# Optimization experiments

Hardware: AMD Instinct MI355X
Metric: run time of the kernel (lower is better)

Reference implementation:

```python
import jax, jax.numpy as jnp
import numpy as np

DIMS = 2048
HEAD_DIM = 64
NUM_HEADS = DIMS // HEAD_DIM   # 32
GQA_HEADS = 2                  # KV heads
EPS = 1e-8


def setup_inputs() -> dict:
    key = jax.random.key(0)
    ks = jax.random.split(key, 6)
    b, s = 2, 2048
    kv_dims = HEAD_DIM * GQA_HEADS  # 128
    x = jax.random.normal(ks[0], (b, s, DIMS), dtype=jnp.float32)
    Wq = jax.random.normal(ks[1], (DIMS, DIMS), dtype=jnp.float32) * 0.02
    Wk = jax.random.normal(ks[2], (kv_dims, DIMS), dtype=jnp.float32) * 0.02
    Wv = jax.random.normal(ks[3], (kv_dims, DIMS), dtype=jnp.float32) * 0.02
    Wo = jax.random.normal(ks[4], (DIMS, DIMS), dtype=jnp.float32) * 0.02
    norm_scale = jnp.ones((DIMS,), dtype=jnp.float32)           # RMSNorm.scale
    split_scale = jnp.full((DIMS,), 0.1, dtype=jnp.float32)     # RMS_split.scale
    return {"x": x, "norm_scale": norm_scale, "split_scale": split_scale,
            "Wq": Wq, "Wk": Wk, "Wv": Wv, "Wo": Wo}


def reference(x, norm_scale, split_scale, Wq, Wk, Wv, Wo):
    b, s, d = x.shape
    H, G, dh = NUM_HEADS, GQA_HEADS, HEAD_DIM
    hpg = H // G  # query heads per KV group

    # RMS_split pre-norm: RMSNorm (l2-norm based) then elementwise scale
    nrm = jnp.linalg.norm(x, axis=-1, keepdims=True) * (d ** -0.5)
    h = (norm_scale * x / (nrm + EPS)) * split_scale

    # projections (nn.Linear with weight [out, in], no bias)
    q = (h @ Wq.T).reshape(b, s, H, dh)          # b s H dh
    k = (h @ Wk.T).reshape(b, s, G, dh)          # b s G dh
    v = (h @ Wv.T).reshape(b, s, G, dh)

    # group query heads: b G hpg s dh
    q = q.transpose(0, 2, 1, 3).reshape(b, G, hpg, s, dh)
    k = k.transpose(0, 2, 1, 3)                  # b G s dh
    v = v.transpose(0, 2, 1, 3)                  # b G s dh

    scores = jnp.einsum('bghsd,bgtd->bghst', q, k) / np.float32(np.sqrt(dh))
    attn = jax.nn.softmax(scores, axis=-1)
    out = jnp.einsum('bghst,bgtd->bghsd', attn, v)   # b G hpg s dh

    out = out.reshape(b, H, s, dh).transpose(0, 2, 1, 3).reshape(b, s, H * dh)
    return x + out @ Wo.T
```

## Files before the change

kernel.cpp:

```cpp
#include <hip/hip_runtime.h>

typedef unsigned short u16;
typedef unsigned int u32;
typedef __bf16 bf16x8 __attribute__((ext_vector_type(8)));
typedef float f32x4 __attribute__((ext_vector_type(4)));

#define DIMS 2048
#define SEQ 2048
#define BATCH 2
#define NH 32
#define NG 2
#define DH 64
#define MROWS (BATCH * SEQ)
#define KVD (NG * DH)

#define SCL2 (0.125f * 1.44269504088896f)

__device__ __forceinline__ u16 f2bf(float f) {
  u32 u = __float_as_uint(f);
  u32 r = u + 0x7fffu + ((u >> 16) & 1u);
  return (u16)(r >> 16);
}
__device__ __forceinline__ u32 pack2(float a, float b) {
  return (u32)f2bf(a) | ((u32)f2bf(b) << 16);
}
__device__ __forceinline__ u32 cvtpk(float a, float b) {
#if __has_builtin(__builtin_amdgcn_cvt_pk_bf16_f32)
  typedef __bf16 bf16x2 __attribute__((ext_vector_type(2)));
  union {
    bf16x2 v;
    u32 u;
  } r;
  r.v = __builtin_amdgcn_cvt_pk_bf16_f32(a, b);
  return r.u;
#else
  return pack2(a, b);
#endif
}
__device__ __forceinline__ void glds16(const u16* g, u16* l) {
  __builtin_amdgcn_global_load_lds(
      (const __attribute__((address_space(1))) void*)g,
      (__attribute__((address_space(3))) void*)l, 16, 0, 0);
}

__global__ __launch_bounds__(256) void rms_split_kernel(
    const float* __restrict__ x, const float* __restrict__ ns,
    const float* __restrict__ ss, u16* __restrict__ h) {
  const int row = blockIdx.x;
  const int tid = threadIdx.x;
  const float* xr = x + (size_t)row * DIMS;
  float4 v0 = ((const float4*)xr)[tid];
  float4 v1 = ((const float4*)xr)[tid + 256];
  float s = v0.x * v0.x + v0.y * v0.y + v0.z * v0.z + v0.w * v0.w +
            v1.x * v1.x + v1.y * v1.y + v1.z * v1.z + v1.w * v1.w;
#pragma unroll
  for (int d = 1; d < 64; d <<= 1) s += __shfl_xor(s, d, 64);
  __shared__ float red[4];
  if ((tid & 63) == 0) red[tid >> 6] = s;
  __syncthreads();
  float tot = red[0] + red[1] + red[2] + red[3];
  float inv = 1.0f / (sqrtf(tot * (1.0f / DIMS)) + 1e-8f);
  float4 a0 = ((const float4*)ns)[tid];
  float4 a1 = ((const float4*)ns)[tid + 256];
  float4 b0 = ((const float4*)ss)[tid];
  float4 b1 = ((const float4*)ss)[tid + 256];
  uint2 o0, o1;
  o0.x = pack2(v0.x * a0.x * b0.x * inv, v0.y * a0.y * b0.y * inv);
  o0.y = pack2(v0.z * a0.z * b0.z * inv, v0.w * a0.w * b0.w * inv);
  o1.x = pack2(v1.x * a1.x * b1.x * inv, v1.y * a1.y * b1.y * inv);
  o1.y = pack2(v1.z * a1.z * b1.z * inv, v1.w * a1.w * b1.w * inv);
  uint2* hr = (uint2*)(h + (size_t)row * DIMS);
  hr[tid] = o0;
  hr[tid + 256] = o1;
}

__global__ __launch_bounds__(256) void cvt4_kernel(
    const float* __restrict__ Wq, const float* __restrict__ Wo,
    const float* __restrict__ Wk, const float* __restrict__ Wv,
    u16* __restrict__ bqkv, u16* __restrict__ bWo) {
  const int bx = blockIdx.x;
  const float* src;
  u16* dst;
  int i;
  if (bx < 4096) {
    src = Wq; dst = bqkv; i = bx;
  } else if (bx < 8192) {
    src = Wo; dst = bWo; i = bx - 4096;
  } else if (bx < 8448) {
    src = Wk; dst = bqkv + (size_t)2048 * 2048; i = bx - 8192;
  } else {
    src = Wv; dst = bqkv + (size_t)2176 * 2048; i = bx - 8448;
  }
  const int idx = i * 256 + threadIdx.x;
  float4 v = ((const float4*)src)[idx];
  uint2 r;
  r.x = pack2(v.x, v.y);
  r.y = pack2(v.z, v.w);
  ((uint2*)dst)[idx] = r;
}

template <int MODE>
__global__ __launch_bounds__(256) void gemm_bt(
    const u16* __restrict__ A, const u16* __restrict__ B, void* __restrict__ Cv,
    const float* __restrict__ R, u16* __restrict__ kb, u16* __restrict__ vtb,
    int M, int N, int K) {
  __shared__ u16 As[2][128 * 32];
  __shared__ u16 Bs[2][128 * 32];
  const int tid = threadIdx.x;
  const int lane = tid & 63;
  const int wv = tid >> 6;
  const int fr = lane & 15;
  const int fq = lane >> 4;
  const int m0 = blockIdx.y * 128;
  const int n0 = blockIdx.x * 128;
  const int wm = wv & 1;
  const int wn = wv >> 1;

  const int srow = tid >> 2;
  const int scol = (tid & 3) * 8;
  const u16* Ag0 = A + (size_t)(m0 + srow) * K + scol;
  const u16* Ag1 = A + (size_t)(m0 + srow + 64) * K + scol;
  const u16* Bg0 = B + (size_t)(n0 + srow) * K + scol;
  const u16* Bg1 = B + (size_t)(n0 + srow + 64) * K + scol;

  f32x4 acc[4][4];
#pragma unroll
  for (int i = 0; i < 4; ++i)
#pragma unroll
    for (int j = 0; j < 4; ++j)
#pragma unroll
      for (int e = 0; e < 4; ++e) acc[i][j][e] = 0.0f;

#define GSTAGE(buf, kk)                            \
  {                                                \
    glds16(Ag0 + (kk), &As[buf][wv * 512]);        \
    glds16(Ag1 + (kk), &As[buf][2048 + wv * 512]); \
    glds16(Bg0 + (kk), &Bs[buf][wv * 512]);        \
    glds16(Bg1 + (kk), &Bs[buf][2048 + wv * 512]); \
  }

#define GCOMP(buf)                                                            \
  {                                                                           \
    bf16x8 af_[4], bf_[4];                                                    \
    _Pragma("unroll") for (int i = 0; i < 4; ++i) {                           \
      af_[i] = *(const bf16x8*)(&As[buf][(wm * 64 + i * 16 + fr) * 32 +       \
                                         fq * 8]);                            \
      bf_[i] = *(const bf16x8*)(&Bs[buf][(wn * 64 + i * 16 + fr) * 32 +       \
                                         fq * 8]);                            \
    }                                                                         \
    _Pragma("unroll") for (int i = 0; i < 4; ++i)                             \
        _Pragma("unroll") for (int j = 0; j < 4; ++j) acc[i][j] =             \
        __builtin_amdgcn_mfma_f32_16x16x32_bf16(af_[i], bf_[j], acc[i][j], 0, \
                                                0, 0);                        \
  }

  GSTAGE(0, 0);
  int k0 = 0;
  for (; k0 + 64 < K; k0 += 64) {
    GSTAGE(1, k0 + 32);
    asm volatile("s_waitcnt vmcnt(4)\ns_barrier" ::: "memory");
    GCOMP(0);
    asm volatile("s_barrier" ::: "memory");
    GSTAGE(0, k0 + 64);
    asm volatile("s_waitcnt vmcnt(4)\ns_barrier" ::: "memory");
    GCOMP(1);
    asm volatile("s_barrier" ::: "memory");
  }
  GSTAGE(1, k0 + 32);
  asm volatile("s_waitcnt vmcnt(4)\ns_barrier" ::: "memory");
  GCOMP(0);
  asm volatile("s_barrier" ::: "memory");
  asm volatile("s_waitcnt vmcnt(0)\ns_barrier" ::: "memory");
  GCOMP(1);
#undef GSTAGE
#undef GCOMP

#pragma unroll
  for (int i = 0; i < 4; ++i) {
    const int m = m0 + wm * 64 + i * 16 + fq * 4;
#pragma unroll
    for (int j = 0; j < 4; ++j) {
      const int n = n0 + wn * 64 + j * 16 + fr;
#pragma unroll
      for (int r = 0; r < 4; ++r) {
        if (MODE == 1) {
          const size_t idx = (size_t)(m + r) * N + n;
          ((float*)Cv)[idx] = R[idx] + acc[i][j][r];
        } else {
          if (n0 < 2048) {
            ((u16*)Cv)[(size_t)(m + r) * DIMS + n] = f2bf(acc[i][j][r]);
          } else {
            const int token = m + r;
            const int bb = token >> 11;
            const int srw = token & 2047;
            const int t = srw >> 6;
            const int rowin = srw & 63;
            if (n0 < 2176) {
              const int d = n - 2048;
              const int gg = d >> 6;
              const int dd = d & 63;
              const int c = ((dd >> 5) << 2) | ((dd >> 3) & 3);
              const int jj = dd & 7;
              const int pos = (rowin & 32) | ((rowin & 4) << 2) |
                              ((rowin & 0x18) >> 1) | (rowin & 3);
              kb[(((size_t)(bb * NG + gg) * 32 + t) * 8 + c) * 512 + pos * 8 +
                 jj] = f2bf(acc[i][j][r] * SCL2);
            } else {
              const int d = n - 2176;
              const int gg = d >> 6;
              const int dv = d & 63;
              const int c = rowin >> 3;
              const int jj = rowin & 7;
              vtb[(((size_t)(bb * NG + gg) * 32 + t) * 8 + c) * 512 + dv * 8 +
                  jj] = f2bf(acc[i][j][r]);
            }
          }
        }
      }
    }
  }
}

__global__ __launch_bounds__(256, 4) void attn_kernel(
    const u16* __restrict__ q, const u16* __restrict__ kbuf,
    const u16* __restrict__ vT, u16* __restrict__ out) {
  __shared__ u16 Ks[2][8 * 512];
  __shared__ u16 Vs[2][8 * 512];
  const int tid = threadIdx.x;
  const int lane = tid & 63;
  const int wv = tid >> 6;
  const int fr = lane & 15;
  const int fq = lane >> 4;
  const int b = blockIdx.x >> 5;
  const int hq = blockIdx.x & 31;
  const int g = hq >> 4;
  const int q0 = blockIdx.y * 128 + wv * 32;

  bf16x8 af[2][2];
#pragma unroll
  for (int mt = 0; mt < 2; ++mt)
#pragma unroll
    for (int kx = 0; kx < 2; ++kx)
      af[mt][kx] =
          *(const bf16x8*)(q + (size_t)(b * SEQ + q0 + mt * 16 + fr) * DIMS +
                           hq * DH + kx * 32 + fq * 8);

  f32x4 Oa[2][4];
  f32x4 On[2];
#pragma unroll
  for (int mt = 0; mt < 2; ++mt) {
#pragma unroll
    for (int e = 0; e < 4; ++e) On[mt][e] = 0.0f;
#pragma unroll
    for (int j = 0; j < 4; ++j)
#pragma unroll
      for (int e = 0; e < 4; ++e) Oa[mt][j][e] = 0.0f;
  }

  bf16x8 onev;
#pragma unroll
  for (int e = 0; e < 8; ++e) onev[e] = (__bf16)1.0f;

  const u16* ksrc = kbuf + (size_t)(b * NG + g) * 32 * 4096;
  const u16* vsrc = vT + (size_t)(b * NG + g) * 32 * 4096;

  const int c0 = wv * 2;
#define STAGE(buf, tile)                                          \
  {                                                               \
    const size_t tb_ = (size_t)(tile)*4096;                       \
    _Pragma("unroll") for (int s = 0; s < 2; ++s) {               \
      const int c = c0 + s;                                       \
      glds16(ksrc + tb_ + c * 512 + lane * 8, &Ks[buf][c * 512]); \
      glds16(vsrc + tb_ + c * 512 + lane * 8, &Vs[buf][c * 512]); \
    }                                                             \
  }

#define COMPUTE(buf)                                                          \
  {                                                                           \
    _Pragma("unroll") for (int kg = 0; kg < 2; ++kg) {                        \
      bf16x8 kf00 = *(const bf16x8*)(&Ks[buf][fq * 512 + (kg * 32 + fr) * 8]); \
      bf16x8 kf01 =                                                           \
          *(const bf16x8*)(&Ks[buf][(4 + fq) * 512 + (kg * 32 + fr) * 8]);    \
      bf16x8 kf10 =                                                           \
          *(const bf16x8*)(&Ks[buf][fq * 512 + (kg * 32 + 16 + fr) * 8]);     \
      bf16x8 kf11 = *(const bf16x8*)(&Ks[buf][(4 + fq) * 512 +                \
                                              (kg * 32 + 16 + fr) * 8]);      \
      bf16x8 vf[4];                                                           \
      _Pragma("unroll") for (int jt = 0; jt < 4; ++jt) vf[jt] =               \
          *(const bf16x8*)(&Vs[buf][(kg * 4 + fq) * 512 + (jt * 16 + fr) * 8]); \
      _Pragma("unroll") for (int mt = 0; mt < 2; ++mt) {                      \
        f32x4 s0 = {0.0f, 0.0f, 0.0f, 0.0f};                                  \
        f32x4 s1 = {0.0f, 0.0f, 0.0f, 0.0f};                                  \
        s0 = __builtin_amdgcn_mfma_f32_16x16x32_bf16(kf00, af[mt][0], s0, 0,  \
                                                     0, 0);                   \
        s0 = __builtin_amdgcn_mfma_f32_16x16x32_bf16(kf01, af[mt][1], s0, 0,  \
                                                     0, 0);                   \
        s1 = __builtin_amdgcn_mfma_f32_16x16x32_bf16(kf10, af[mt][0], s1, 0,  \
                                                     0, 0);                   \
        s1 = __builtin_amdgcn_mfma_f32_16x16x32_bf16(kf11, af[mt][1], s1, 0,  \
                                                     0, 0);                   \
        const float p0 = __builtin_amdgcn_exp2f(s0[0]);                       \
        const float p1 = __builtin_amdgcn_exp2f(s0[1]);                       \
        const float p2 = __builtin_amdgcn_exp2f(s0[2]);                       \
        const float p3 = __builtin_amdgcn_exp2f(s0[3]);                       \
        const float p4 = __builtin_amdgcn_exp2f(s1[0]);                       \
        const float p5 = __builtin_amdgcn_exp2f(s1[1]);                       \
        const float p6 = __builtin_amdgcn_exp2f(s1[2]);                       \
        const float p7 = __builtin_amdgcn_exp2f(s1[3]);                       \
        union {                                                               \
          bf16x8 v;                                                           \
          u32 u[4];                                                           \
        } pu;                                                                 \
        pu.u[0] = cvtpk(p0, p1);                                              \
        pu.u[1] = cvtpk(p2, p3);                                              \
        pu.u[2] = cvtpk(p4, p5);                                              \
        pu.u[3] = cvtpk(p6, p7);                                              \
        _Pragma("unroll") for (int jt = 0; jt < 4; ++jt) Oa[mt][jt] =         \
            __builtin_amdgcn_mfma_f32_16x16x32_bf16(pu.v, vf[jt], Oa[mt][jt], \
                                                    0, 0, 0);                 \
        On[mt] = __builtin_amdgcn_mfma_f32_16x16x32_bf16(pu.v, onev, On[mt],  \
                                                         0, 0, 0);            \
      }                                                                       \
    }                                                                         \
  }

  STAGE(0, 0);
  for (int it = 0; it < 32; it += 2) {
    STAGE(1, (it + 1) & 31);
    asm volatile("s_waitcnt vmcnt(4)\ns_barrier" ::: "memory");
    COMPUTE(0);
    asm volatile("s_barrier" ::: "memory");
    STAGE(0, (it + 2) & 31);
    asm volatile("s_waitcnt vmcnt(4)\ns_barrier" ::: "memory");
    COMPUTE(1);
    asm volatile("s_barrier" ::: "memory");
  }
#undef STAGE
#undef COMPUTE

#pragma unroll
  for (int mt = 0; mt < 2; ++mt)
#pragma unroll
    for (int r = 0; r < 4; ++r) {
      const float invl = 1.0f / On[mt][r];
      const int row = q0 + mt * 16 + fq * 4 + r;
#pragma unroll
      for (int jt = 0; jt < 4; ++jt)
        out[(size_t)(b * SEQ + row) * DIMS + hq * DH + jt * 16 + fr] =
            f2bf(Oa[mt][jt][r] * invl);
    }
}

extern "C" void kernel_launch(void* const* d_in, const int* in_sizes, int n_in,
                              void* d_out, int out_size, void* d_ws,
                              size_t ws_size, hipStream_t stream) {
  const float* x = (const float*)d_in[0];
  const float* ns = (const float*)d_in[1];
  const float* ssc = (const float*)d_in[2];
  const float* Wq = (const float*)d_in[3];
  const float* Wk = (const float*)d_in[4];
  const float* Wv = (const float*)d_in[5];
  const float* Wo = (const float*)d_in[6];

  char* ws = (char*)d_ws;
  u16* hbuf = (u16*)(ws);
  u16* bqkv = (u16*)(ws + 16777216);
  u16* bWo = (u16*)(ws + 26214400);
  u16* qb = (u16*)(ws + 34603008);
  u16* kb = (u16*)(ws + 51380224);
  u16* vtb = (u16*)(ws + 52428800);
  u16* ab = (u16*)(ws + 53477376);

  rms_split_kernel<<<dim3(4096), dim3(256), 0, stream>>>(x, ns, ssc, hbuf);
  cvt4_kernel<<<dim3(8704), dim3(256), 0, stream>>>(Wq, Wo, Wk, Wv, bqkv, bWo);

  gemm_bt<2><<<dim3(18, 32), dim3(256), 0, stream>>>(
      hbuf, bqkv, qb, nullptr, kb, vtb, 4096, 2048, 2048);
  attn_kernel<<<dim3(64, 16), dim3(256), 0, stream>>>(qb, kb, vtb, ab);
  gemm_bt<1><<<dim3(16, 32), dim3(256), 0, stream>>>(
      ab, bWo, d_out, x, nullptr, nullptr, 4096, 2048, 2048);
}
```

Before: 299.8 us.

## Widen GEMM K-tile with swizzled LDS, XCD block remap, fuse prep kernels

```diff
diff --git a/kernel.cpp b/kernel.cpp
--- a/kernel.cpp
+++ b/kernel.cpp
@@ -43,60 +43,60 @@
       (__attribute__((address_space(3))) void*)l, 16, 0, 0);
 }
 
-__global__ __launch_bounds__(256) void rms_split_kernel(
+__global__ __launch_bounds__(256) void prep_kernel(
     const float* __restrict__ x, const float* __restrict__ ns,
-    const float* __restrict__ ss, u16* __restrict__ h) {
-  const int row = blockIdx.x;
-  const int tid = threadIdx.x;
-  const float* xr = x + (size_t)row * DIMS;
-  float4 v0 = ((const float4*)xr)[tid];
-  float4 v1 = ((const float4*)xr)[tid + 256];
-  float s = v0.x * v0.x + v0.y * v0.y + v0.z * v0.z + v0.w * v0.w +
-            v1.x * v1.x + v1.y * v1.y + v1.z * v1.z + v1.w * v1.w;
-#pragma unroll
-  for (int d = 1; d < 64; d <<= 1) s += __shfl_xor(s, d, 64);
-  __shared__ float red[4];
-  if ((tid & 63) == 0) red[tid >> 6] = s;
-  __syncthreads();
-  float tot = red[0] + red[1] + red[2] + red[3];
-  float inv = 1.0f / (sqrtf(tot * (1.0f / DIMS)) + 1e-8f);
-  float4 a0 = ((const float4*)ns)[tid];
-  float4 a1 = ((const float4*)ns)[tid + 256];
-  float4 b0 = ((const float4*)ss)[tid];
-  float4 b1 = ((const float4*)ss)[tid + 256];
-  uint2 o0, o1;
-  o0.x = pack2(v0.x * a0.x * b0.x * inv, v0.y * a0.y * b0.y * inv);
-  o0.y = pack2(v0.z * a0.z * b0.z * inv, v0.w * a0.w * b0.w * inv);
-  o1.x = pack2(v1.x * a1.x * b1.x * inv, v1.y * a1.y * b1.y * inv);
-  o1.y = pack2(v1.z * a1.z * b1.z * inv, v1.w * a1.w * b1.w * inv);
-  uint2* hr = (uint2*)(h + (size_t)row * DIMS);
-  hr[tid] = o0;
-  hr[tid + 256] = o1;
-}
-
-__global__ __launch_bounds__(256) void cvt4_kernel(
+    const float* __restrict__ ss, u16* __restrict__ h,
     const float* __restrict__ Wq, const float* __restrict__ Wo,
     const float* __restrict__ Wk, const float* __restrict__ Wv,
     u16* __restrict__ bqkv, u16* __restrict__ bWo) {
   const int bx = blockIdx.x;
-  const float* src;
-  u16* dst;
-  int i;
+  const int tid = threadIdx.x;
   if (bx < 4096) {
-    src = Wq; dst = bqkv; i = bx;
-  } else if (bx < 8192) {
-    src = Wo; dst = bWo; i = bx - 4096;
-  } else if (bx < 8448) {
-    src = Wk; dst = bqkv + (size_t)2048 * 2048; i = bx - 8192;
+    const float* xr = x + (size_t)bx * DIMS;
+    float4 v0 = ((const float4*)xr)[tid];
+    float4 v1 = ((const float4*)xr)[tid + 256];
+    float s = v0.x * v0.x + v0.y * v0.y + v0.z * v0.z + v0.w * v0.w +
+              v1.x * v1.x + v1.y * v1.y + v1.z * v1.z + v1.w * v1.w;
+#pragma unroll
+    for (int d = 1; d < 64; d <<= 1) s += __shfl_xor(s, d, 64);
+    __shared__ float red[4];
+    if ((tid & 63) == 0) red[tid >> 6] = s;
+    __syncthreads();
+    float tot = red[0] + red[1] + red[2] + red[3];
+    float inv = 1.0f / (sqrtf(tot * (1.0f / DIMS)) + 1e-8f);
+    float4 a0 = ((const float4*)ns)[tid];
+    float4 a1 = ((const float4*)ns)[tid + 256];
+    float4 b0 = ((const float4*)ss)[tid];
+    float4 b1 = ((const float4*)ss)[tid + 256];
+    uint2 o0, o1;
+    o0.x = pack2(v0.x * a0.x * b0.x * inv, v0.y * a0.y * b0.y * inv);
+    o0.y = pack2(v0.z * a0.z * b0.z * inv, v0.w * a0.w * b0.w * inv);
+    o1.x = pack2(v1.x * a1.x * b1.x * inv, v1.y * a1.y * b1.y * inv);
+    o1.y = pack2(v1.z * a1.z * b1.z * inv, v1.w * a1.w * b1.w * inv);
+    uint2* hr = (uint2*)(h + (size_t)bx * DIMS);
+    hr[tid] = o0;
+    hr[tid + 256] = o1;
   } else {
-    src = Wv; dst = bqkv + (size_t)2176 * 2048; i = bx - 8448;
-  }
-  const int idx = i * 256 + threadIdx.x;
-  float4 v = ((const float4*)src)[idx];
-  uint2 r;
-  r.x = pack2(v.x, v.y);
-  r.y = pack2(v.z, v.w);
-  ((uint2*)dst)[idx] = r;
+    const int cx = bx - 4096;
+    const float* src;
+    u16* dst;
+    int i;
+    if (cx < 4096) {
+      src = Wq; dst = bqkv; i = cx;
+    } else if (cx < 8192) {
+      src = Wo; dst = bWo; i = cx - 4096;
+    } else if (cx < 8448) {
+      src = Wk; dst = bqkv + (size_t)2048 * 2048; i = cx - 8192;
+    } else {
+      src = Wv; dst = bqkv + (size_t)2176 * 2048; i = cx - 8448;
+    }
+    const int idx = i * 256 + tid;
+    float4 v = ((const float4*)src)[idx];
+    uint2 r;
+    r.x = pack2(v.x, v.y);
+    r.y = pack2(v.z, v.w);
+    ((uint2*)dst)[idx] = r;
+  }
 }
 
 template <int MODE>
@@ -104,24 +104,34 @@
     const u16* __restrict__ A, const u16* __restrict__ B, void* __restrict__ Cv,
     const float* __restrict__ R, u16* __restrict__ kb, u16* __restrict__ vtb,
     int M, int N, int K) {
-  __shared__ u16 As[2][128 * 32];
-  __shared__ u16 Bs[2][128 * 32];
+  __shared__ u16 As[2][128 * 64];
+  __shared__ u16 Bs[2][128 * 64];
   const int tid = threadIdx.x;
   const int lane = tid & 63;
   const int wv = tid >> 6;
   const int fr = lane & 15;
   const int fq = lane >> 4;
-  const int m0 = blockIdx.y * 128;
-  const int n0 = blockIdx.x * 128;
+
+  const int gx = gridDim.x;
+  const int nwg = gx * gridDim.y;
+  const int id = blockIdx.y * gx + blockIdx.x;
+  const int cpx = nwg >> 3;
+  const int sid = (id & 7) * cpx + (id >> 3);
+  const int m0 = (sid / gx) * 128;
+  const int n0 = (sid % gx) * 128;
+
   const int wm = wv & 1;
   const int wn = wv >> 1;
 
-  const int srow = tid >> 2;
-  const int scol = (tid & 3) * 8;
-  const u16* Ag0 = A + (size_t)(m0 + srow) * K + scol;
-  const u16* Ag1 = A + (size_t)(m0 + srow + 64) * K + scol;
-  const u16* Bg0 = B + (size_t)(n0 + srow) * K + scol;
-  const u16* Bg1 = B + (size_t)(n0 + srow + 64) * K + scol;
+  const int srow = tid >> 3;
+  const int scol = (((tid & 7) ^ ((tid >> 3) & 7)) << 3);
+  const u16* Ag[4];
+  const u16* Bg[4];
+#pragma unroll
+  for (int i = 0; i < 4; ++i) {
+    Ag[i] = A + (size_t)(m0 + i * 32 + srow) * K + scol;
+    Bg[i] = B + (size_t)(n0 + i * 32 + srow) * K + scol;
+  }
 
   f32x4 acc[4][4];
 #pragma unroll
@@ -131,43 +141,47 @@
 #pragma unroll
       for (int e = 0; e < 4; ++e) acc[i][j][e] = 0.0f;
 
-#define GSTAGE(buf, kk)                            \
-  {                                                \
-    glds16(Ag0 + (kk), &As[buf][wv * 512]);        \
-    glds16(Ag1 + (kk), &As[buf][2048 + wv * 512]); \
-    glds16(Bg0 + (kk), &Bs[buf][wv * 512]);        \
-    glds16(Bg1 + (kk), &Bs[buf][2048 + wv * 512]); \
+#define GSTAGE(buf, kk0)                                  \
+  {                                                       \
+    _Pragma("unroll") for (int i = 0; i < 4; ++i) {       \
+      glds16(Ag[i] + (kk0), &As[buf][i * 2048 + wv * 512]); \
+      glds16(Bg[i] + (kk0), &Bs[buf][i * 2048 + wv * 512]); \
+    }                                                     \
   }
 
 #define GCOMP(buf)                                                            \
   {                                                                           \
-    bf16x8 af_[4], bf_[4];                                                    \
-    _Pragma("unroll") for (int i = 0; i < 4; ++i) {                           \
-      af_[i] = *(const bf16x8*)(&As[buf][(wm * 64 + i * 16 + fr) * 32 +       \
-                                         fq * 8]);                            \
-      bf_[i] = *(const bf16x8*)(&Bs[buf][(wn * 64 + i * 16 + fr) * 32 +       \
-                                         fq * 8]);                            \
+    _Pragma("unroll") for (int kk = 0; kk < 2; ++kk) {                        \
+      bf16x8 af_[4], bf_[4];                                                  \
+      _Pragma("unroll") for (int i = 0; i < 4; ++i) {                         \
+        af_[i] = *(const bf16x8*)(&As[buf][(wm * 64 + i * 16 + fr) * 64 +     \
+                                           ((((kk << 2) | fq) ^ (fr & 7))     \
+                                            << 3)]);                          \
+        bf_[i] = *(const bf16x8*)(&Bs[buf][(wn * 64 + i * 16 + fr) * 64 +     \
+                                           ((((kk << 2) | fq) ^ (fr & 7))     \
+                                            << 3)]);                          \
+      }                                                                       \
+      _Pragma("unroll") for (int i = 0; i < 4; ++i)                           \
+          _Pragma("unroll") for (int j = 0; j < 4; ++j) acc[i][j] =           \
+          __builtin_amdgcn_mfma_f32_16x16x32_bf16(af_[i], bf_[j], acc[i][j],  \
+                                                  0, 0, 0);                   \
     }                                                                         \
-    _Pragma("unroll") for (int i = 0; i < 4; ++i)                             \
-        _Pragma("unroll") for (int j = 0; j < 4; ++j) acc[i][j] =             \
-        __builtin_amdgcn_mfma_f32_16x16x32_bf16(af_[i], bf_[j], acc[i][j], 0, \
-                                                0, 0);                        \
   }
 
   GSTAGE(0, 0);
   int k0 = 0;
-  for (; k0 + 64 < K; k0 += 64) {
-    GSTAGE(1, k0 + 32);
-    asm volatile("s_waitcnt vmcnt(4)\ns_barrier" ::: "memory");
+  for (; k0 + 128 < K; k0 += 128) {
+    GSTAGE(1, k0 + 64);
+    asm volatile("s_waitcnt vmcnt(8)\ns_barrier" ::: "memory");
     GCOMP(0);
     asm volatile("s_barrier" ::: "memory");
-    GSTAGE(0, k0 + 64);
-    asm volatile("s_waitcnt vmcnt(4)\ns_barrier" ::: "memory");
+    GSTAGE(0, k0 + 128);
+    asm volatile("s_waitcnt vmcnt(8)\ns_barrier" ::: "memory");
     GCOMP(1);
     asm volatile("s_barrier" ::: "memory");
   }
-  GSTAGE(1, k0 + 32);
-  asm volatile("s_waitcnt vmcnt(4)\ns_barrier" ::: "memory");
+  GSTAGE(1, k0 + 64);
+  asm volatile("s_waitcnt vmcnt(8)\ns_barrier" ::: "memory");
   GCOMP(0);
   asm volatile("s_barrier" ::: "memory");
   asm volatile("s_waitcnt vmcnt(0)\ns_barrier" ::: "memory");
@@ -371,8 +385,8 @@
   u16* vtb = (u16*)(ws + 52428800);
   u16* ab = (u16*)(ws + 53477376);
 
-  rms_split_kernel<<<dim3(4096), dim3(256), 0, stream>>>(x, ns, ssc, hbuf);
-  cvt4_kernel<<<dim3(8704), dim3(256), 0, stream>>>(Wq, Wo, Wk, Wv, bqkv, bWo);
+  prep_kernel<<<dim3(12800), dim3(256), 0, stream>>>(x, ns, ssc, hbuf, Wq, Wo,
+                                                     Wk, Wv, bqkv, bWo);
 
   gemm_bt<2><<<dim3(18, 32), dim3(256), 0, stream>>>(
       hbuf, bqkv, qb, nullptr, kb, vtb, 4096, 2048, 2048);
```

After: 294.3 us. About the same (-1.8%).
